# Optimization experiments

Hardware: AMD Instinct MI355X
Metric: run time of the kernel (lower is better)

Reference implementation:

```python
import jax, jax.numpy as jnp
import numpy as np


def _sage(x_src, x_dst, src, dst, Wl, bl, Wr, num_dst):
    # PyG SAGEConv with mean aggregation: lin_l(mean_{j->i} x_src[j]) + lin_r(x_dst[i])
    msg = x_src[src]                                   # [E, d] gather
    agg = jax.ops.segment_sum(msg, dst, num_segments=num_dst)          # [Nd, d]
    cnt = jax.ops.segment_sum(jnp.ones_like(dst, dtype=x_src.dtype), dst,
                              num_segments=num_dst)                     # [Nd]
    mean = agg / jnp.maximum(cnt, 1.0)[:, None]
    return mean @ Wl + bl + x_dst @ Wr                 # [Nd, d_out]


def setup_inputs() -> dict:
    key = jax.random.key(0)
    ks = jax.random.split(key, 16)
    Na, Nb, E, D = 200000, 100000, 500000, 128
    s = 1.0 / np.sqrt(D)
    inp = {
        'x_a': jax.random.normal(ks[0], (Na, D), jnp.float32),
        'x_b': jax.random.normal(ks[1], (Nb, D), jnp.float32),
        'e0_src': jax.random.randint(ks[2], (E,), 0, Na, jnp.int32),
        'e0_dst': jax.random.randint(ks[3], (E,), 0, Na, jnp.int32),
        'e1_src': jax.random.randint(ks[4], (E,), 0, Na, jnp.int32),
        'e1_dst': jax.random.randint(ks[5], (E,), 0, Nb, jnp.int32),
        'e2_src': jax.random.randint(ks[6], (E,), 0, Nb, jnp.int32),
        'e2_dst': jax.random.randint(ks[7], (E,), 0, Na, jnp.int32),
        'Wl0': jax.random.normal(ks[8], (D, D), jnp.float32) * s,
        'bl0': jnp.zeros((D,), jnp.float32),
        'Wr0': jax.random.normal(ks[9], (D, D), jnp.float32) * s,
        'Wl1': jax.random.normal(ks[10], (D, D), jnp.float32) * s,
        'bl1': jnp.zeros((D,), jnp.float32),
        'Wr1': jax.random.normal(ks[11], (D, D), jnp.float32) * s,
        'Wl2': jax.random.normal(ks[12], (D, D), jnp.float32) * s,
        'bl2': jnp.zeros((D,), jnp.float32),
        'Wr2': jax.random.normal(ks[13], (D, D), jnp.float32) * s,
        'rel_logits': jnp.zeros((3,), jnp.float32),
    }
    return inp


def reference(x_a, x_b, e0_src, e0_dst, e1_src, e1_dst, e2_src, e2_dst,
              Wl0, bl0, Wr0, Wl1, bl1, Wr1, Wl2, bl2, Wr2, rel_logits):
    Na, Nb = x_a.shape[0], x_b.shape[0]
    rw = jax.nn.softmax(rel_logits)
    # relation 0: a -> a (self node type), 1: a -> b, 2: b -> a
    h0 = _sage(x_a, x_a, e0_src, e0_dst, Wl0, bl0, Wr0, Na)
    h1 = _sage(x_a, x_b, e1_src, e1_dst, Wl1, bl1, Wr1, Nb)
    h2 = _sage(x_b, x_a, e2_src, e2_dst, Wl2, bl2, Wr2, Na)
    out_a = rw[0] * h0 + rw[2] * h2
    out_b = rw[1] * h1
    return out_a, out_b, rw
```

## Files before the change

kernel.cpp:

```cpp
#include <hip/hip_runtime.h>
#include <hip/hip_bf16.h>

#define DD 128
#define CAP02 16
#define CAP1 32
#define OVFC 4096

typedef float f32x4 __attribute__((ext_vector_type(4)));
typedef __bf16 bf16x8 __attribute__((ext_vector_type(8)));

__global__ void prep_kernel(const float* __restrict__ Wl0, const float* __restrict__ bl0, const float* __restrict__ Wr0,
                            const float* __restrict__ Wl1, const float* __restrict__ bl1, const float* __restrict__ Wr1,
                            const float* __restrict__ Wl2, const float* __restrict__ bl2, const float* __restrict__ Wr2,
                            const float* __restrict__ rl,
                            __bf16* __restrict__ WtA, __bf16* __restrict__ Wtb,
                            float* __restrict__ ba, float* __restrict__ bb,
                            float* __restrict__ rw_out) {
    const int n = threadIdx.x;
    float l0 = rl[0], l1 = rl[1], l2 = rl[2];
    float mx = fmaxf(l0, fmaxf(l1, l2));
    float e0 = expf(l0 - mx), e1 = expf(l1 - mx), e2 = expf(l2 - mx);
    float s = e0 + e1 + e2;
    float r0 = e0 / s, r1 = e1 / s, r2 = e2 / s;
    for (int k = 0; k < DD; k++) {
        WtA[n * 384 + k]       = (__bf16)(r0 * Wl0[k * DD + n]);
        WtA[n * 384 + 128 + k] = (__bf16)(r0 * Wr0[k * DD + n] + r2 * Wr2[k * DD + n]);
        WtA[n * 384 + 256 + k] = (__bf16)(r2 * Wl2[k * DD + n]);
        Wtb[n * 256 + k]       = (__bf16)(r1 * Wl1[k * DD + n]);
        Wtb[n * 256 + 128 + k] = (__bf16)(r1 * Wr1[k * DD + n]);
    }
    ba[n] = r0 * bl0[n] + r2 * bl2[n];
    bb[n] = r1 * bl1[n];
    if (n < 3) rw_out[n] = (n == 0 ? r0 : (n == 1 ? r1 : r2));
}

__global__ __launch_bounds__(256) void fill_bucket(const int* __restrict__ src, const int* __restrict__ dst,
                                                   int E, int Nd, int Ns, int cap,
                                                   int* __restrict__ cnt, int* __restrict__ bucket,
                                                   int* __restrict__ ovf_cnt, int2* __restrict__ ovf) {
    int e = blockIdx.x * 256 + threadIdx.x;
    if (e >= E) return;
    int d = dst[e];
    if (d < 0 || d >= Nd) return;
    int s = src[e];
    if (s < 0 || s >= Ns) return;
    int slot = atomicAdd(&cnt[d], 1);
    if (slot < cap) bucket[(size_t)d * cap + slot] = s;
    else { int o = atomicAdd(ovf_cnt, 1); if (o < OVFC) ovf[o] = make_int2(d, s); }
}

template <int KSRC>
__global__ __launch_bounds__(64) void fused_tile(const float* __restrict__ XA,
                                                 const float* __restrict__ XB,
                                                 const float* __restrict__ XR,
                                                 const int* __restrict__ C0, const int* __restrict__ BK0, int cap0,
                                                 const int* __restrict__ C2, const int* __restrict__ BK2, int cap2,
                                                 const __bf16* __restrict__ Wt,
                                                 const float* __restrict__ bias,
                                                 float* __restrict__ out, int Nrows) {
    constexpr int K = KSRC * 128;
    constexpr int KP = K + 8;
    __shared__ __bf16 A[16 * KP];
    const int lane = threadIdx.x;
    const int t = blockIdx.x;
    const int c2 = lane * 2;

    for (int r = 0; r < 16; r++) {
        const int row = t * 16 + r;
        if (row >= Nrows) {
            A[r * KP + c2] = (__bf16)0.f; A[r * KP + c2 + 1] = (__bf16)0.f;
            A[r * KP + 128 + c2] = (__bf16)0.f; A[r * KP + 128 + c2 + 1] = (__bf16)0.f;
            if (KSRC == 3) { A[r * KP + 256 + c2] = (__bf16)0.f; A[r * KP + 256 + c2 + 1] = (__bf16)0.f; }
            continue;
        }
        {
            const int d = C0[row];
            const int du = d < cap0 ? d : cap0;
            const float sc = 1.0f / fmaxf((float)d, 1.0f);
            const int* bk = BK0 + (size_t)row * cap0;
            float ax = 0.f, ay = 0.f;
            for (int i = 0; i < du; i++) {
                const float2 v = ((const float2*)(XA + (size_t)bk[i] * DD))[lane];
                ax += v.x; ay += v.y;
            }
            A[r * KP + c2] = (__bf16)(ax * sc);
            A[r * KP + c2 + 1] = (__bf16)(ay * sc);
        }
        {
            const float2 v = ((const float2*)(XR + (size_t)row * DD))[lane];
            A[r * KP + 128 + c2] = (__bf16)v.x;
            A[r * KP + 128 + c2 + 1] = (__bf16)v.y;
        }
        if (KSRC == 3) {
            const int d = C2[row];
            const int du = d < cap2 ? d : cap2;
            const float sc = 1.0f / fmaxf((float)d, 1.0f);
            const int* bk = BK2 + (size_t)row * cap2;
            float ax = 0.f, ay = 0.f;
            for (int i = 0; i < du; i++) {
                const float2 v = ((const float2*)(XB + (size_t)bk[i] * DD))[lane];
                ax += v.x; ay += v.y;
            }
            A[r * KP + 256 + c2] = (__bf16)(ax * sc);
            A[r * KP + 256 + c2 + 1] = (__bf16)(ay * sc);
        }
    }
    __syncthreads();

    const int m = lane & 15;
    const int g = lane >> 4;
    f32x4 acc[8];
#pragma unroll
    for (int n = 0; n < 8; n++) acc[n] = (f32x4)0.0f;
#pragma unroll
    for (int ks = 0; ks < K / 32; ks++) {
        const int koff = ks * 32 + g * 8;
        const bf16x8 a = *(const bf16x8*)(&A[m * KP + koff]);
#pragma unroll
        for (int n = 0; n < 8; n++) {
            const bf16x8 b = *(const bf16x8*)(Wt + (size_t)(n * 16 + m) * K + koff);
            acc[n] = __builtin_amdgcn_mfma_f32_16x16x32_bf16(a, b, acc[n], 0, 0, 0);
        }
    }

#pragma unroll
    for (int n = 0; n < 8; n++) {
        const int col = n * 16 + m;
        const float bv = bias[col];
#pragma unroll
        for (int r = 0; r < 4; r++) {
            const int orow = t * 16 + g * 4 + r;
            if (orow < Nrows) out[(size_t)orow * DD + col] = acc[n][r] + bv;
        }
    }
}

__global__ __launch_bounds__(128) void ovf_fix(const int* __restrict__ ovfc, const int2* __restrict__ ovf,
                                               const float* __restrict__ x, const int* __restrict__ cnt,
                                               const __bf16* __restrict__ Wt, int K, int sec,
                                               float* __restrict__ out) {
    int m = *ovfc;
    if (m > OVFC) m = OVFC;
    const int n = threadIdx.x;
    for (int i = blockIdx.x; i < m; i += gridDim.x) {
        const int2 p = ovf[i];
        const float sc = 1.0f / fmaxf((float)cnt[p.x], 1.0f);
        float acc = 0.f;
        for (int k = 0; k < DD; k++)
            acc += x[(size_t)p.y * DD + k] * (float)Wt[(size_t)n * K + sec + k];
        atomicAdd(&out[(size_t)p.x * DD + n], acc * sc);
    }
}

static inline int imin(int a, int b) { return a < b ? a : b; }

extern "C" void kernel_launch(void* const* d_in, const int* in_sizes, int n_in,
                              void* d_out, int out_size, void* d_ws, size_t ws_size,
                              hipStream_t stream) {
    if (n_in != 18) return;

    const float* x_a = (const float*)d_in[0];
    const float* x_b = (const float*)d_in[1];
    const int* e0_src = (const int*)d_in[2];
    const int* e0_dst = (const int*)d_in[3];
    const int* e1_src = (const int*)d_in[4];
    const int* e1_dst = (const int*)d_in[5];
    const int* e2_src = (const int*)d_in[6];
    const int* e2_dst = (const int*)d_in[7];
    const float* Wl0 = (const float*)d_in[8];
    const float* bl0 = (const float*)d_in[9];
    const float* Wr0 = (const float*)d_in[10];
    const float* Wl1 = (const float*)d_in[11];
    const float* bl1 = (const float*)d_in[12];
    const float* Wr1 = (const float*)d_in[13];
    const float* Wl2 = (const float*)d_in[14];
    const float* bl2 = (const float*)d_in[15];
    const float* Wr2 = (const float*)d_in[16];
    const float* rl  = (const float*)d_in[17];

    const int Na = in_sizes[0] / DD;
    const int Nb = in_sizes[1] / DD;
    const int E0 = in_sizes[2], E1 = in_sizes[4], E2 = in_sizes[6];

    float* out_f = (float*)d_out;
    float* out_a = out_f;
    float* out_b = out_f + (size_t)Na * DD;
    float* rw_out = out_f + (size_t)Na * DD + (size_t)Nb * DD;

    char* base = (char*)d_ws;
    size_t off = 0;
    auto alloc = [&](size_t bytes) { char* r = base + off; off += (bytes + 511) & ~(size_t)511; return r; };
    int* cnt0 = (int*)alloc((size_t)Na * 4);
    int* cnt1 = (int*)alloc((size_t)Nb * 4);
    int* cnt2 = (int*)alloc((size_t)Na * 4);
    int* ovfc = (int*)alloc(512);
    int2* ovf0 = (int2*)alloc(OVFC * 8);
    int2* ovf1 = (int2*)alloc(OVFC * 8);
    int2* ovf2 = (int2*)alloc(OVFC * 8);
    size_t zero_hi = off;
    __bf16* WtA = (__bf16*)alloc(128 * 384 * 2);
    __bf16* Wtb = (__bf16*)alloc(128 * 256 * 2);
    float* ba = (float*)alloc(512);
    float* bb = (float*)alloc(512);
    size_t b0cap = (size_t)Na * CAP02;
    size_t b1cap = (size_t)Nb * CAP1;
    int* bucket0 = (int*)alloc((b0cap > b1cap ? b0cap : b1cap) * 4);
    int* bucket2 = (int*)alloc((size_t)Na * CAP02 * 4);
    int* bucket1 = bucket0;
    if (ws_size < off) return;

    hipMemsetAsync(d_ws, 0, zero_hi, stream);
    prep_kernel<<<1, 128, 0, stream>>>(Wl0, bl0, Wr0, Wl1, bl1, Wr1, Wl2, bl2, Wr2, rl,
                                       WtA, Wtb, ba, bb, rw_out);

    const int fb0 = (E0 + 255) / 256, fb1 = (E1 + 255) / 256, fb2 = (E2 + 255) / 256;

    fill_bucket<<<fb1, 256, 0, stream>>>(e1_src, e1_dst, E1, Nb, Na, CAP1, cnt1, bucket1, ovfc + 1, ovf1);
    fused_tile<2><<<(Nb + 15) / 16, 64, 0, stream>>>(x_a, nullptr, x_b,
                                                     cnt1, bucket1, CAP1,
                                                     nullptr, nullptr, 0,
                                                     Wtb, bb, out_b, Nb);
    ovf_fix<<<32, 128, 0, stream>>>(ovfc + 1, ovf1, x_a, cnt1, Wtb, 256, 0, out_b);

    fill_bucket<<<fb0, 256, 0, stream>>>(e0_src, e0_dst, E0, Na, Na, CAP02, cnt0, bucket0, ovfc + 0, ovf0);
    fill_bucket<<<fb2, 256, 0, stream>>>(e2_src, e2_dst, E2, Na, Nb, CAP02, cnt2, bucket2, ovfc + 2, ovf2);
    fused_tile<3><<<(Na + 15) / 16, 64, 0, stream>>>(x_a, x_b, x_a,
                                                     cnt0, bucket0, CAP02,
                                                     cnt2, bucket2, CAP02,
                                                     WtA, ba, out_a, Na);
    ovf_fix<<<32, 128, 0, stream>>>(ovfc + 0, ovf0, x_a, cnt0, WtA, 384, 0, out_a);
    ovf_fix<<<32, 128, 0, stream>>>(ovfc + 2, ovf2, x_b, cnt2, WtA, 384, 256, out_a);
}
```

Baseline: 609.0 us.

## Pack four waves per block and stream K sections through a smaller LDS tile

The fused gather+MFMA kernel now runs four independent 16-row tiles per 256-thread block instead of one tile per 64-thread block. Each wave fills a single 128-wide K section into LDS and accumulates it with MFMA before moving to the next section, so LDS per tile drops from the full K width to 128 columns. The goal is higher occupancy and fewer blocks for the latency-bound random-row gathers. In exchange, block-wide __syncthreads couple the four waves, so a wave whose rows have many neighbours holds back the other three.

```diff
diff --git a/kernel.cpp b/kernel.cpp
--- a/kernel.cpp
+++ b/kernel.cpp
@@ -50,87 +50,85 @@
 }
 
 template <int KSRC>
-__global__ __launch_bounds__(64) void fused_tile(const float* __restrict__ XA,
-                                                 const float* __restrict__ XB,
-                                                 const float* __restrict__ XR,
-                                                 const int* __restrict__ C0, const int* __restrict__ BK0, int cap0,
-                                                 const int* __restrict__ C2, const int* __restrict__ BK2, int cap2,
-                                                 const __bf16* __restrict__ Wt,
-                                                 const float* __restrict__ bias,
-                                                 float* __restrict__ out, int Nrows) {
+__global__ __launch_bounds__(256) void fused_tile(const float* __restrict__ XA,
+                                                  const float* __restrict__ XB,
+                                                  const float* __restrict__ XR,
+                                                  const int* __restrict__ C0, const int* __restrict__ BK0, int cap0,
+                                                  const int* __restrict__ C2, const int* __restrict__ BK2, int cap2,
+                                                  const __bf16* __restrict__ Wt,
+                                                  const float* __restrict__ bias,
+                                                  float* __restrict__ out, int Nrows) {
     constexpr int K = KSRC * 128;
-    constexpr int KP = K + 8;
-    __shared__ __bf16 A[16 * KP];
-    const int lane = threadIdx.x;
-    const int t = blockIdx.x;
+    constexpr int KP = 136;
+    __shared__ __bf16 A[4][16 * KP];
+    const int w = threadIdx.x >> 6;
+    const int lane = threadIdx.x & 63;
+    __bf16* Aw = A[w];
+    const int t = blockIdx.x * 4 + w;
+    const bool active = (t * 16 < Nrows);
     const int c2 = lane * 2;
-
-    for (int r = 0; r < 16; r++) {
-        const int row = t * 16 + r;
-        if (row >= Nrows) {
-            A[r * KP + c2] = (__bf16)0.f; A[r * KP + c2 + 1] = (__bf16)0.f;
-            A[r * KP + 128 + c2] = (__bf16)0.f; A[r * KP + 128 + c2 + 1] = (__bf16)0.f;
-            if (KSRC == 3) { A[r * KP + 256 + c2] = (__bf16)0.f; A[r * KP + 256 + c2 + 1] = (__bf16)0.f; }
-            continue;
+    const int m = lane & 15, g = lane >> 4;
+
+    f32x4 acc[8];
+#pragma unroll
+    for (int n = 0; n < 8; n++) acc[n] = (f32x4)0.0f;
+
+#pragma unroll
+    for (int sec = 0; sec < KSRC; sec++) {
+        if (active) {
+            for (int r = 0; r < 16; r++) {
+                const int row = t * 16 + r;
+                float ax = 0.f, ay = 0.f;
+                if (row < Nrows) {
+                    if (sec == 1) {
+                        const float2 v = ((const float2*)(XR + (size_t)row * DD))[lane];
+                        ax = v.x; ay = v.y;
+                    } else {
+                        const int* cnt = (sec == 0) ? C0 : C2;
+                        const int* bkp = (sec == 0) ? BK0 : BK2;
+                        const int cap  = (sec == 0) ? cap0 : cap2;
+                        const float* X = (sec == 0) ? XA : XB;
+                        const int d = cnt[row];
+                        const int du = d < cap ? d : cap;
+                        const float sc = 1.0f / fmaxf((float)d, 1.0f);
+                        const int* bk = bkp + (size_t)row * cap;
+                        for (int i = 0; i < du; i++) {
+                            const float2 v = ((const float2*)(X + (size_t)bk[i] * DD))[lane];
+                            ax += v.x; ay += v.y;
+                        }
+                        ax *= sc; ay *= sc;
+                    }
+                }
+                Aw[r * KP + c2] = (__bf16)ax;
+                Aw[r * KP + c2 + 1] = (__bf16)ay;
+            }
         }
-        {
-            const int d = C0[row];
-            const int du = d < cap0 ? d : cap0;
-            const float sc = 1.0f / fmaxf((float)d, 1.0f);
-            const int* bk = BK0 + (size_t)row * cap0;
-            float ax = 0.f, ay = 0.f;
-            for (int i = 0; i < du; i++) {
-                const float2 v = ((const float2*)(XA + (size_t)bk[i] * DD))[lane];
-                ax += v.x; ay += v.y;
+        __syncthreads();
+        if (active) {
+#pragma unroll
+            for (int ks = 0; ks < 4; ks++) {
+                const int koff = ks * 32 + g * 8;
+                const bf16x8 a = *(const bf16x8*)(&Aw[m * KP + koff]);
+#pragma unroll
+                for (int n = 0; n < 8; n++) {
+                    const bf16x8 b = *(const bf16x8*)(Wt + (size_t)(n * 16 + m) * K + sec * 128 + koff);
+                    acc[n] = __builtin_amdgcn_mfma_f32_16x16x32_bf16(a, b, acc[n], 0, 0, 0);
+                }
             }
-            A[r * KP + c2] = (__bf16)(ax * sc);
-            A[r * KP + c2 + 1] = (__bf16)(ay * sc);
         }
-        {
-            const float2 v = ((const float2*)(XR + (size_t)row * DD))[lane];
-            A[r * KP + 128 + c2] = (__bf16)v.x;
-            A[r * KP + 128 + c2 + 1] = (__bf16)v.y;
-        }
-        if (KSRC == 3) {
-            const int d = C2[row];
-            const int du = d < cap2 ? d : cap2;
-            const float sc = 1.0f / fmaxf((float)d, 1.0f);
-            const int* bk = BK2 + (size_t)row * cap2;
-            float ax = 0.f, ay = 0.f;
-            for (int i = 0; i < du; i++) {
-                const float2 v = ((const float2*)(XB + (size_t)bk[i] * DD))[lane];
-                ax += v.x; ay += v.y;
+        __syncthreads();
+    }
+
+    if (active) {
+#pragma unroll
+        for (int n = 0; n < 8; n++) {
+            const int col = n * 16 + m;
+            const float bv = bias[col];
+#pragma unroll
+            for (int r = 0; r < 4; r++) {
+                const int orow = t * 16 + g * 4 + r;
+                if (orow < Nrows) out[(size_t)orow * DD + col] = acc[n][r] + bv;
             }
-            A[r * KP + 256 + c2] = (__bf16)(ax * sc);
-            A[r * KP + 256 + c2 + 1] = (__bf16)(ay * sc);
-        }
-    }
-    __syncthreads();
-
-    const int m = lane & 15;
-    const int g = lane >> 4;
-    f32x4 acc[8];
-#pragma unroll
-    for (int n = 0; n < 8; n++) acc[n] = (f32x4)0.0f;
-#pragma unroll
-    for (int ks = 0; ks < K / 32; ks++) {
-        const int koff = ks * 32 + g * 8;
-        const bf16x8 a = *(const bf16x8*)(&A[m * KP + koff]);
-#pragma unroll
-        for (int n = 0; n < 8; n++) {
-            const bf16x8 b = *(const bf16x8*)(Wt + (size_t)(n * 16 + m) * K + koff);
-            acc[n] = __builtin_amdgcn_mfma_f32_16x16x32_bf16(a, b, acc[n], 0, 0, 0);
-        }
-    }
-
-#pragma unroll
-    for (int n = 0; n < 8; n++) {
-        const int col = n * 16 + m;
-        const float bv = bias[col];
-#pragma unroll
-        for (int r = 0; r < 4; r++) {
-            const int orow = t * 16 + g * 4 + r;
-            if (orow < Nrows) out[(size_t)orow * DD + col] = acc[n][r] + bv;
         }
     }
 }
@@ -151,8 +149,6 @@
         atomicAdd(&out[(size_t)p.x * DD + n], acc * sc);
     }
 }
-
-static inline int imin(int a, int b) { return a < b ? a : b; }
 
 extern "C" void kernel_launch(void* const* d_in, const int* in_sizes, int n_in,
                               void* d_out, int out_size, void* d_ws, size_t ws_size,
@@ -216,18 +212,18 @@
     const int fb0 = (E0 + 255) / 256, fb1 = (E1 + 255) / 256, fb2 = (E2 + 255) / 256;
 
     fill_bucket<<<fb1, 256, 0, stream>>>(e1_src, e1_dst, E1, Nb, Na, CAP1, cnt1, bucket1, ovfc + 1, ovf1);
-    fused_tile<2><<<(Nb + 15) / 16, 64, 0, stream>>>(x_a, nullptr, x_b,
-                                                     cnt1, bucket1, CAP1,
-                                                     nullptr, nullptr, 0,
-                                                     Wtb, bb, out_b, Nb);
+    fused_tile<2><<<(Nb + 63) / 64, 256, 0, stream>>>(x_a, nullptr, x_b,
+                                                      cnt1, bucket1, CAP1,
+                                                      nullptr, nullptr, 0,
+                                                      Wtb, bb, out_b, Nb);
     ovf_fix<<<32, 128, 0, stream>>>(ovfc + 1, ovf1, x_a, cnt1, Wtb, 256, 0, out_b);
 
     fill_bucket<<<fb0, 256, 0, stream>>>(e0_src, e0_dst, E0, Na, Na, CAP02, cnt0, bucket0, ovfc + 0, ovf0);
     fill_bucket<<<fb2, 256, 0, stream>>>(e2_src, e2_dst, E2, Na, Nb, CAP02, cnt2, bucket2, ovfc + 2, ovf2);
-    fused_tile<3><<<(Na + 15) / 16, 64, 0, stream>>>(x_a, x_b, x_a,
-                                                     cnt0, bucket0, CAP02,
-                                                     cnt2, bucket2, CAP02,
-                                                     WtA, ba, out_a, Na);
+    fused_tile<3><<<(Na + 63) / 64, 256, 0, stream>>>(x_a, x_b, x_a,
+                                                      cnt0, bucket0, CAP02,
+                                                      cnt2, bucket2, CAP02,
+                                                      WtA, ba, out_a, Na);
     ovf_fix<<<32, 128, 0, stream>>>(ovfc + 0, ovf0, x_a, cnt0, WtA, 384, 0, out_a);
     ovf_fix<<<32, 128, 0, stream>>>(ovfc + 2, ovf2, x_b, cnt2, WtA, 384, 256, out_a);
 }
```

After: 708.2 us. 1.16x slower.
